# Performance work log

Hardware: AMD Instinct MI355X
Metric: run time of the kernel (lower is better)

Reference implementation:

```python
import jax, jax.numpy as jnp
import numpy as np

EPS = 1e-6
DELTA = 1e-6
GAMMA = 1.0


def setup_inputs() -> dict:
    key = jax.random.key(0)
    ks = jax.random.split(key, 6)
    B, N, D, DDIR, DSIM = 2, 384, 256, 128, 64
    sc = lambda d: 1.0 / np.sqrt(d)
    return {
        "t": jax.random.normal(ks[0], (B, N, D), jnp.float32),
        "Qd": jax.random.normal(ks[1], (D, DDIR), jnp.float32) * sc(D),
        "Kd": jax.random.normal(ks[2], (D, DDIR), jnp.float32) * sc(D),
        "Vd": jax.random.normal(ks[3], (DDIR, D), jnp.float32) * sc(DDIR),
        "Qs": jax.random.normal(ks[4], (D, DSIM), jnp.float32) * sc(D),
        "Ks": jax.random.normal(ks[5], (D, DSIM), jnp.float32) * sc(D),
        "a_l": jnp.ones((1,), jnp.float32),
        "b_l": jnp.zeros((1,), jnp.float32),
    }


def reference(t, Qd, Kd, Vd, Qs, Ks, a_l, b_l):
    B, N, D = t.shape
    d_sim = Qs.shape[1]
    # --- similarity: s_ij = <Qs t_i, Ks t_j>/sqrt(d_sim), then symmetrize ---
    q = t @ Qs  # (B,N,d_sim)
    k = t @ Ks
    s = jnp.einsum('bnd,bmd->bnm', q, k) / jnp.sqrt(jnp.float32(d_sim))
    s = 0.5 * (s + s.transpose(0, 2, 1))
    # --- global z-score over off-diagonal entries (biased var) ---
    eye = jnp.eye(N, dtype=bool)[None]  # (1,N,N)
    cnt = jnp.float32(N * (N - 1))
    mu = jnp.where(eye, 0.0, s).sum((1, 2), keepdims=True) / cnt  # (B,1,1)
    var = jnp.where(eye, 0.0, (s - mu) ** 2).sum((1, 2), keepdims=True) / cnt
    s_hat = (s - mu) / jnp.sqrt(var + EPS)
    tilde_s = a_l.reshape(-1, 1, 1) * s_hat + b_l.reshape(-1, 1, 1)
    # --- gates / mass / inertia / apportioned step ---
    A = jax.nn.sigmoid(tilde_s)                                  # (B,N,N)
    m = 1.0 / (jnp.exp(GAMMA * tilde_s).sum(axis=2) + EPS)       # (B,N)
    w = A * m[:, None, :]                                        # w_ij = m_j A_ij
    alpha = A * (w / (w.sum(axis=2, keepdims=True) + DELTA))     # (B,N,N)
    # --- antisymmetric Hadamard direction gate ---
    qd = t @ Qd  # (B,N,d_dir)
    kd = t @ Kd
    had = qd[:, :, None, :] * kd[:, None, :, :]                  # (B,N,N,d_dir)
    kappa = jnp.einsum('bijr,rd->bijd', had, Vd)                 # (B,N,N,D)
    gate = jax.nn.sigmoid(kappa - kappa.transpose(0, 2, 1, 3))
    Dpair = gate * (t[:, :, None, :] - t[:, None, :, :])         # D_ij = gate*(t_i - t_j)
    # --- exclude self pairs, aggregate update ---
    off = ~eye  # (1,N,N)
    alpha = jnp.where(off, alpha, 0.0)
    Dpair = jnp.where(off[..., None], Dpair, 0.0)
    t_next = t - jnp.einsum('bnm,bnmd->bnd', alpha, Dpair)
    return t_next
```

## Files before the change

### kernel.cpp

```cpp
#include <hip/hip_runtime.h>

#define Bn 2
#define Nn 384
#define Dn 256
#define Rn 128
#define Sn 64
#define BNn (Bn*Nn)
#define NEG_LOG2E -1.44269504088896f

typedef short short8 __attribute__((ext_vector_type(8)));
typedef float f32x4 __attribute__((ext_vector_type(4)));
typedef unsigned int uint;
typedef unsigned short ushort;

static __device__ __forceinline__ float fast_sigmoid(float x) {
    return __builtin_amdgcn_rcpf(1.0f + __expf(-x));
}
static __device__ __forceinline__ ushort f2bf(float f) {
    uint u = __float_as_uint(f);
    uint r = (u + 0x7fffu + ((u >> 16) & 1u)) >> 16;
    return (ushort)r;
}
static __device__ __forceinline__ float bf2f(ushort u) {
    return __uint_as_float(((uint)u) << 16);
}

__global__ __launch_bounds__(256)
void prep_kernel(const float* __restrict__ t,
                 const float* __restrict__ Qd, const float* __restrict__ Kd,
                 const float* __restrict__ Vd,
                 const float* __restrict__ Qs, const float* __restrict__ Ks,
                 float* __restrict__ q, float* __restrict__ k,
                 ushort* __restrict__ qdb, ushort* __restrict__ kdb,
                 ushort* __restrict__ VdT, float* __restrict__ stats) {
    const int bi = blockIdx.x;
    const int tid = threadIdx.x;
    if (bi >= 192) {
        const int idx = (bi - 192) * 256 + tid;
        const int d = idx >> 7, r = idx & 127;
        VdT[idx] = f2bf(NEG_LOG2E * Vd[(size_t)r * Dn + d]);
        if (bi == 319 && tid < 4) stats[tid] = 0.0f;
        return;
    }
    __shared__ float trow[4][Dn];
    const int r0 = bi * 4;
    for (int idx = tid; idx < 4 * Dn; idx += 256)
        trow[idx >> 8][idx & 255] = t[(size_t)r0 * Dn + idx];
    __syncthreads();
    {
        const float* W = (tid < 128) ? Qd : Kd;
        ushort* ob = (tid < 128) ? qdb : kdb;
        const int col = tid & 127;
        float a0 = 0.f, a1 = 0.f, a2 = 0.f, a3 = 0.f;
        for (int kk = 0; kk < Dn; kk += 4) {
            float4 t0 = *(const float4*)&trow[0][kk];
            float4 t1 = *(const float4*)&trow[1][kk];
            float4 t2 = *(const float4*)&trow[2][kk];
            float4 t3 = *(const float4*)&trow[3][kk];
            float w0 = W[(size_t)(kk + 0) * 128 + col];
            float w1 = W[(size_t)(kk + 1) * 128 + col];
            float w2 = W[(size_t)(kk + 2) * 128 + col];
            float w3 = W[(size_t)(kk + 3) * 128 + col];
            a0 += t0.x * w0 + t0.y * w1 + t0.z * w2 + t0.w * w3;
            a1 += t1.x * w0 + t1.y * w1 + t1.z * w2 + t1.w * w3;
            a2 += t2.x * w0 + t2.y * w1 + t2.z * w2 + t2.w * w3;
            a3 += t3.x * w0 + t3.y * w1 + t3.z * w2 + t3.w * w3;
        }
        ob[(size_t)(r0 + 0) * 128 + col] = f2bf(a0);
        ob[(size_t)(r0 + 1) * 128 + col] = f2bf(a1);
        ob[(size_t)(r0 + 2) * 128 + col] = f2bf(a2);
        ob[(size_t)(r0 + 3) * 128 + col] = f2bf(a3);
    }
    if (tid < 128) {
        const float* W = (tid < 64) ? Qs : Ks;
        float* of = (tid < 64) ? q : k;
        const int col = tid & 63;
        float a0 = 0.f, a1 = 0.f, a2 = 0.f, a3 = 0.f;
        for (int kk = 0; kk < Dn; kk += 4) {
            float4 t0 = *(const float4*)&trow[0][kk];
            float4 t1 = *(const float4*)&trow[1][kk];
            float4 t2 = *(const float4*)&trow[2][kk];
            float4 t3 = *(const float4*)&trow[3][kk];
            float w0 = W[(size_t)(kk + 0) * 64 + col];
            float w1 = W[(size_t)(kk + 1) * 64 + col];
            float w2 = W[(size_t)(kk + 2) * 64 + col];
            float w3 = W[(size_t)(kk + 3) * 64 + col];
            a0 += t0.x * w0 + t0.y * w1 + t0.z * w2 + t0.w * w3;
            a1 += t1.x * w0 + t1.y * w1 + t1.z * w2 + t1.w * w3;
            a2 += t2.x * w0 + t2.y * w1 + t2.z * w2 + t2.w * w3;
            a3 += t3.x * w0 + t3.y * w1 + t3.z * w2 + t3.w * w3;
        }
        of[(size_t)(r0 + 0) * 64 + col] = a0;
        of[(size_t)(r0 + 1) * 64 + col] = a1;
        of[(size_t)(r0 + 2) * 64 + col] = a2;
        of[(size_t)(r0 + 3) * 64 + col] = a3;
    }
}

__global__ __launch_bounds__(256)
void ssym_kernel(const float* __restrict__ q, const float* __restrict__ k,
                 float* __restrict__ ssym, float* __restrict__ stats) {
    __shared__ float qi[16][68], ki[16][68], qj[16][68], kj[16][68];
    __shared__ float red[256];
    const int b = blockIdx.z, it = blockIdx.x, jt = blockIdx.y;
    const int tid = threadIdx.x;
    const int r0 = tid >> 6, c = tid & 63;
#pragma unroll
    for (int p = 0; p < 4; ++p) {
        int row = r0 + 4 * p;
        qi[row][c] = q[((size_t)(b * Nn + it * 16 + row)) * Sn + c];
        ki[row][c] = k[((size_t)(b * Nn + it * 16 + row)) * Sn + c];
        qj[row][c] = q[((size_t)(b * Nn + jt * 16 + row)) * Sn + c];
        kj[row][c] = k[((size_t)(b * Nn + jt * 16 + row)) * Sn + c];
    }
    __syncthreads();
    const int ti = tid >> 4, tj = tid & 15;
    float acc = 0.0f;
#pragma unroll
    for (int dd = 0; dd < Sn; dd += 4) {
        float4 a  = *(const float4*)&qi[ti][dd];
        float4 bb = *(const float4*)&kj[tj][dd];
        float4 cc = *(const float4*)&qj[tj][dd];
        float4 d  = *(const float4*)&ki[ti][dd];
        acc += a.x * bb.x + a.y * bb.y + a.z * bb.z + a.w * bb.w
             + cc.x * d.x + cc.y * d.y + cc.z * d.z + cc.w * d.w;
    }
    const float sval = acc * 0.0625f;
    const int gi = it * 16 + ti, gj = jt * 16 + tj;
    ssym[((size_t)(b * Nn + gi)) * Nn + gj] = sval;
    const float v = (gi == gj) ? 0.0f : sval;

    red[tid] = v;
    __syncthreads();
    for (int off = 128; off > 0; off >>= 1) {
        if (tid < off) red[tid] += red[tid + off];
        __syncthreads();
    }
    const float tot_s = red[0];
    __syncthreads();
    red[tid] = v * v;
    __syncthreads();
    for (int off = 128; off > 0; off >>= 1) {
        if (tid < off) red[tid] += red[tid + off];
        __syncthreads();
    }
    if (tid == 0) {
        atomicAdd(&stats[b * 2 + 0], tot_s);
        atomicAdd(&stats[b * 2 + 1], red[0]);
    }
}

__global__ __launch_bounds__(256)
void m_kernel(const float* __restrict__ ssym, const float* __restrict__ stats,
              const float* __restrict__ a_l, const float* __restrict__ b_l,
              const float* __restrict__ t, float* __restrict__ out,
              float* __restrict__ m) {
    __shared__ float red[256];
    const int row = blockIdx.x;
    const int b = row / Nn;
    const float cnt_inv = 1.0f / (float)(Nn * (Nn - 1));
    const float mu = stats[b * 2 + 0] * cnt_inv;
    const float var = stats[b * 2 + 1] * cnt_inv - mu * mu;
    const float isg = rsqrtf(var + 1e-6f);
    const float a = a_l[0], bbias = b_l[0];
    const int tid = threadIdx.x;
    out[(size_t)row * Dn + tid] = t[(size_t)row * Dn + tid];
    float sum = __expf(a * (ssym[(size_t)row * Nn + tid] - mu) * isg + bbias);
    if (tid < 128)
        sum += __expf(a * (ssym[(size_t)row * Nn + 256 + tid] - mu) * isg + bbias);
    red[tid] = sum;
    __syncthreads();
    for (int off = 128; off > 0; off >>= 1) {
        if (tid < off) red[tid] += red[tid + off];
        __syncthreads();
    }
    if (tid == 0) m[row] = 1.0f / (red[0] + 1e-6f);
}

__global__ __launch_bounds__(256, 3)
void pair_kernel(const float* __restrict__ t, const float* __restrict__ ssym,
                 const float* __restrict__ mptr, const float* __restrict__ stats,
                 const float* __restrict__ a_l, const float* __restrict__ b_l,
                 const ushort* __restrict__ qdb, const ushort* __restrict__ kdb,
                 const ushort* __restrict__ VdT, float* __restrict__ out) {
    __shared__ ushort h_s[128][136];
    __shared__ float alpha_s[Nn];
    __shared__ float qdi_s[Rn], kdi_s[Rn];
    __shared__ float red[256];

    const int bx = blockIdx.x;
    const int tile = bx / BNn;
    const int bi = bx - tile * BNn;
    const int jt0 = tile * 128;
    const int b = bi / Nn;
    const int i = bi - b * Nn;
    const int tid = threadIdx.x;
    const int wave = tid >> 6, lane = tid & 63;
    const int ln = lane & 15, quad = lane >> 4;
    const int wd0 = wave * 64;

    if (tid < Rn) {
        qdi_s[tid] = bf2f(qdb[(size_t)bi * Rn + tid]);
        kdi_s[tid] = bf2f(kdb[(size_t)bi * Rn + tid]);
    }

    {
        const float cnt_inv = 1.0f / (float)(Nn * (Nn - 1));
        const float mu = stats[b * 2 + 0] * cnt_inv;
        const float var = stats[b * 2 + 1] * cnt_inv - mu * mu;
        const float isg = rsqrtf(var + 1e-6f);
        const float a = a_l[0], bbias = b_l[0];
        float A0, am0, A1 = 0.f, am1 = 0.f;
        {
            float s0 = ssym[(size_t)bi * Nn + tid];
            A0 = fast_sigmoid(a * (s0 - mu) * isg + bbias);
            am0 = A0 * mptr[b * Nn + tid];
        }
        if (tid < 128) {
            float s1 = ssym[(size_t)bi * Nn + 256 + tid];
            A1 = fast_sigmoid(a * (s1 - mu) * isg + bbias);
            am1 = A1 * mptr[b * Nn + 256 + tid];
        }
        red[tid] = am0 + am1;
        __syncthreads();
        for (int off = 128; off > 0; off >>= 1) {
            if (tid < off) red[tid] += red[tid + off];
            __syncthreads();
        }
        const float inv = 1.0f / (red[0] + 1e-6f);
        alpha_s[tid] = (tid == i) ? 0.f : A0 * am0 * inv;
        if (tid < 128)
            alpha_s[256 + tid] = ((256 + tid) == i) ? 0.f : A1 * am1 * inv;
    }

    {
        const int jj = tid >> 1;
        const int r0s = (tid & 1) * 64;
        const size_t rowj = (size_t)(b * Nn + jt0 + jj) * Rn;
        const uint4* qp = (const uint4*)(qdb + rowj + r0s);
        const uint4* kp = (const uint4*)(kdb + rowj + r0s);
#pragma unroll
        for (int c = 0; c < 8; ++c) {
            uint4 qv = qp[c], kv = kp[c];
            uint pk[4];
#pragma unroll
            for (int p = 0; p < 4; ++p) {
                uint qu = (&qv.x)[p], ku = (&kv.x)[p];
                float qlo = __uint_as_float(qu << 16);
                float qhi = __uint_as_float(qu & 0xffff0000u);
                float klo = __uint_as_float(ku << 16);
                float khi = __uint_as_float(ku & 0xffff0000u);
                const int r = r0s + c * 8 + p * 2;
                float h0 = qdi_s[r]     * klo - kdi_s[r]     * qlo;
                float h1 = qdi_s[r + 1] * khi - kdi_s[r + 1] * qhi;
                pk[p] = (uint)f2bf(h0) | ((uint)f2bf(h1) << 16);
            }
            uint4 w; w.x = pk[0]; w.y = pk[1]; w.z = pk[2]; w.w = pk[3];
            *(uint4*)&h_s[jj][r0s + c * 8] = w;
        }
    }

    short8 vf[4][4];
#pragma unroll
    for (int dt = 0; dt < 4; ++dt)
#pragma unroll
        for (int ks = 0; ks < 4; ++ks)
            vf[dt][ks] = *(const short8*)&VdT[(size_t)(wd0 + dt * 16 + ln) * Rn + ks * 32 + quad * 8];

    float4 tiv[4];
#pragma unroll
    for (int dt = 0; dt < 4; ++dt)
        tiv[dt] = *(const float4*)&t[(size_t)bi * Dn + wd0 + dt * 16 + quad * 4];

    float4 outac[4];
#pragma unroll
    for (int dt = 0; dt < 4; ++dt) outac[dt] = make_float4(0.f, 0.f, 0.f, 0.f);

    __syncthreads();

#pragma unroll 1
    for (int jsub = 0; jsub < 8; ++jsub) {
        short8 hf[4];
#pragma unroll
        for (int ks = 0; ks < 4; ++ks)
            hf[ks] = *(const short8*)&h_s[jsub * 16 + ln][ks * 32 + quad * 8];
        const int j = jt0 + jsub * 16 + ln;
        const float al = alpha_s[j];
        const size_t trow_ = (size_t)(b * Nn + j) * Dn;
        float4 tjv[4];
#pragma unroll
        for (int dt = 0; dt < 4; ++dt)
            tjv[dt] = *(const float4*)&t[trow_ + wd0 + dt * 16 + quad * 4];

        f32x4 aA[4], aB[4];
#pragma unroll
        for (int dt = 0; dt < 4; ++dt) {
            f32x4 x = {0.f, 0.f, 0.f, 0.f}, y = {0.f, 0.f, 0.f, 0.f};
            x = __builtin_amdgcn_mfma_f32_16x16x32_bf16(vf[dt][0], hf[0], x, 0, 0, 0);
            y = __builtin_amdgcn_mfma_f32_16x16x32_bf16(vf[dt][1], hf[1], y, 0, 0, 0);
            x = __builtin_amdgcn_mfma_f32_16x16x32_bf16(vf[dt][2], hf[2], x, 0, 0, 0);
            y = __builtin_amdgcn_mfma_f32_16x16x32_bf16(vf[dt][3], hf[3], y, 0, 0, 0);
            aA[dt] = x; aB[dt] = y;
        }
#pragma unroll
        for (int dt = 0; dt < 4; ++dt) {
            const float4 tj = tjv[dt];
            float e0 = aA[dt][0] + aB[dt][0];
            float e1 = aA[dt][1] + aB[dt][1];
            float e2 = aA[dt][2] + aB[dt][2];
            float e3 = aA[dt][3] + aB[dt][3];
            float g0 = __builtin_amdgcn_rcpf(1.0f + __builtin_amdgcn_exp2f(e0));
            float g1 = __builtin_amdgcn_rcpf(1.0f + __builtin_amdgcn_exp2f(e1));
            float g2 = __builtin_amdgcn_rcpf(1.0f + __builtin_amdgcn_exp2f(e2));
            float g3 = __builtin_amdgcn_rcpf(1.0f + __builtin_amdgcn_exp2f(e3));
            outac[dt].x += al * g0 * (tiv[dt].x - tj.x);
            outac[dt].y += al * g1 * (tiv[dt].y - tj.y);
            outac[dt].z += al * g2 * (tiv[dt].z - tj.z);
            outac[dt].w += al * g3 * (tiv[dt].w - tj.w);
        }
    }

#pragma unroll
    for (int dt = 0; dt < 4; ++dt) {
        float4 v = outac[dt];
#pragma unroll
        for (int mask = 1; mask < 16; mask <<= 1) {
            v.x += __shfl_xor(v.x, mask);
            v.y += __shfl_xor(v.y, mask);
            v.z += __shfl_xor(v.z, mask);
            v.w += __shfl_xor(v.w, mask);
        }
        if (ln == 0) {
            float* op = &out[(size_t)bi * Dn + wd0 + dt * 16 + quad * 4];
            atomicAdd(op + 0, -v.x);
            atomicAdd(op + 1, -v.y);
            atomicAdd(op + 2, -v.z);
            atomicAdd(op + 3, -v.w);
        }
    }
}

extern "C" void kernel_launch(void* const* d_in, const int* in_sizes, int n_in,
                              void* d_out, int out_size, void* d_ws, size_t ws_size,
                              hipStream_t stream) {
    const float* t   = (const float*)d_in[0];
    const float* Qd  = (const float*)d_in[1];
    const float* Kd  = (const float*)d_in[2];
    const float* Vd  = (const float*)d_in[3];
    const float* Qs  = (const float*)d_in[4];
    const float* Ks  = (const float*)d_in[5];
    const float* a_l = (const float*)d_in[6];
    const float* b_l = (const float*)d_in[7];
    float* out = (float*)d_out;
    float* ws  = (float*)d_ws;

    float* q     = ws;
    float* k     = q + BNn * Sn;
    float* ssym  = k + BNn * Sn;
    float* m     = ssym + (size_t)BNn * Nn;
    float* stats = m + BNn;
    ushort* qdb  = (ushort*)(stats + 8);
    ushort* kdb  = qdb + (size_t)BNn * Rn;
    ushort* VdT  = kdb + (size_t)BNn * Rn;

    hipLaunchKernelGGL(prep_kernel, dim3(320), dim3(256), 0, stream,
                       t, Qd, Kd, Vd, Qs, Ks, q, k, qdb, kdb, VdT, stats);
    hipLaunchKernelGGL(ssym_kernel, dim3(Nn / 16, Nn / 16, Bn), dim3(256), 0, stream,
                       q, k, ssym, stats);
    hipLaunchKernelGGL(m_kernel, dim3(BNn), dim3(256), 0, stream,
                       ssym, stats, a_l, b_l, t, out, m);
    hipLaunchKernelGGL(pair_kernel, dim3(3 * BNn), dim3(256), 0, stream,
                       t, ssym, m, stats, a_l, b_l, qdb, kdb, VdT, out);
}
```

Before: 191.9 us.

## Precompute alpha row denominators in separate kernel and halve pair-kernel j-tile

Adds a wden_kernel that computes each row's inverse normalizer of sum_j A_ij m_j once, instead of every pair-kernel block recomputing the full 384-wide row reduction. The pair kernel then computes alpha only for its own 64-column tile. The tile shrinks from 128 to 64 columns, giving twice as many blocks with less shared memory and a higher occupancy hint. The cost is an extra kernel launch and reloading the per-block i-row state (VdT fragments, t_i) across twice as many blocks.

```diff
diff --git a/kernel.cpp b/kernel.cpp
--- a/kernel.cpp
+++ b/kernel.cpp
@@ -177,21 +177,54 @@
     if (tid == 0) m[row] = 1.0f / (red[0] + 1e-6f);
 }
 
-__global__ __launch_bounds__(256, 3)
+__global__ __launch_bounds__(256)
+void wden_kernel(const float* __restrict__ ssym, const float* __restrict__ stats,
+                 const float* __restrict__ a_l, const float* __restrict__ b_l,
+                 const float* __restrict__ m, float* __restrict__ invden) {
+    __shared__ float red[256];
+    const int row = blockIdx.x;
+    const int b = row / Nn;
+    const float cnt_inv = 1.0f / (float)(Nn * (Nn - 1));
+    const float mu = stats[b * 2 + 0] * cnt_inv;
+    const float var = stats[b * 2 + 1] * cnt_inv - mu * mu;
+    const float isg = rsqrtf(var + 1e-6f);
+    const float a = a_l[0], bbias = b_l[0];
+    const int tid = threadIdx.x;
+    float wsum;
+    {
+        float s0 = ssym[(size_t)row * Nn + tid];
+        float A0 = fast_sigmoid(a * (s0 - mu) * isg + bbias);
+        wsum = A0 * m[b * Nn + tid];
+    }
+    if (tid < 128) {
+        float s1 = ssym[(size_t)row * Nn + 256 + tid];
+        float A1 = fast_sigmoid(a * (s1 - mu) * isg + bbias);
+        wsum += A1 * m[b * Nn + 256 + tid];
+    }
+    red[tid] = wsum;
+    __syncthreads();
+    for (int off = 128; off > 0; off >>= 1) {
+        if (tid < off) red[tid] += red[tid + off];
+        __syncthreads();
+    }
+    if (tid == 0) invden[row] = 1.0f / (red[0] + 1e-6f);
+}
+
+__global__ __launch_bounds__(256, 6)
 void pair_kernel(const float* __restrict__ t, const float* __restrict__ ssym,
                  const float* __restrict__ mptr, const float* __restrict__ stats,
                  const float* __restrict__ a_l, const float* __restrict__ b_l,
+                 const float* __restrict__ invden,
                  const ushort* __restrict__ qdb, const ushort* __restrict__ kdb,
                  const ushort* __restrict__ VdT, float* __restrict__ out) {
-    __shared__ ushort h_s[128][136];
-    __shared__ float alpha_s[Nn];
+    __shared__ ushort h_s[64][136];
+    __shared__ float alpha_s[64];
     __shared__ float qdi_s[Rn], kdi_s[Rn];
-    __shared__ float red[256];
 
     const int bx = blockIdx.x;
     const int tile = bx / BNn;
     const int bi = bx - tile * BNn;
-    const int jt0 = tile * 128;
+    const int jt0 = tile * 64;
     const int b = bi / Nn;
     const int i = bi - b * Nn;
     const int tid = threadIdx.x;
@@ -203,44 +236,29 @@
         qdi_s[tid] = bf2f(qdb[(size_t)bi * Rn + tid]);
         kdi_s[tid] = bf2f(kdb[(size_t)bi * Rn + tid]);
     }
-
-    {
+    if (tid >= 192) {
+        const int jl = tid - 192;
+        const int j = jt0 + jl;
         const float cnt_inv = 1.0f / (float)(Nn * (Nn - 1));
         const float mu = stats[b * 2 + 0] * cnt_inv;
         const float var = stats[b * 2 + 1] * cnt_inv - mu * mu;
         const float isg = rsqrtf(var + 1e-6f);
         const float a = a_l[0], bbias = b_l[0];
-        float A0, am0, A1 = 0.f, am1 = 0.f;
-        {
-            float s0 = ssym[(size_t)bi * Nn + tid];
-            A0 = fast_sigmoid(a * (s0 - mu) * isg + bbias);
-            am0 = A0 * mptr[b * Nn + tid];
-        }
-        if (tid < 128) {
-            float s1 = ssym[(size_t)bi * Nn + 256 + tid];
-            A1 = fast_sigmoid(a * (s1 - mu) * isg + bbias);
-            am1 = A1 * mptr[b * Nn + 256 + tid];
-        }
-        red[tid] = am0 + am1;
-        __syncthreads();
-        for (int off = 128; off > 0; off >>= 1) {
-            if (tid < off) red[tid] += red[tid + off];
-            __syncthreads();
-        }
-        const float inv = 1.0f / (red[0] + 1e-6f);
-        alpha_s[tid] = (tid == i) ? 0.f : A0 * am0 * inv;
-        if (tid < 128)
-            alpha_s[256 + tid] = ((256 + tid) == i) ? 0.f : A1 * am1 * inv;
-    }
+        float s = ssym[(size_t)bi * Nn + j];
+        float A = fast_sigmoid(a * (s - mu) * isg + bbias);
+        float al = A * A * mptr[b * Nn + j] * invden[bi];
+        alpha_s[jl] = (j == i) ? 0.f : al;
+    }
+    __syncthreads();
 
     {
-        const int jj = tid >> 1;
-        const int r0s = (tid & 1) * 64;
+        const int jj = tid >> 2;
+        const int r0s = (tid & 3) * 32;
         const size_t rowj = (size_t)(b * Nn + jt0 + jj) * Rn;
         const uint4* qp = (const uint4*)(qdb + rowj + r0s);
         const uint4* kp = (const uint4*)(kdb + rowj + r0s);
 #pragma unroll
-        for (int c = 0; c < 8; ++c) {
+        for (int c = 0; c < 4; ++c) {
             uint4 qv = qp[c], kv = kp[c];
             uint pk[4];
 #pragma unroll
@@ -279,13 +297,13 @@
     __syncthreads();
 
 #pragma unroll 1
-    for (int jsub = 0; jsub < 8; ++jsub) {
+    for (int jsub = 0; jsub < 4; ++jsub) {
         short8 hf[4];
 #pragma unroll
         for (int ks = 0; ks < 4; ++ks)
             hf[ks] = *(const short8*)&h_s[jsub * 16 + ln][ks * 32 + quad * 8];
         const int j = jt0 + jsub * 16 + ln;
-        const float al = alpha_s[j];
+        const float al = alpha_s[jsub * 16 + ln];
         const size_t trow_ = (size_t)(b * Nn + j) * Dn;
         float4 tjv[4];
 #pragma unroll
@@ -354,14 +372,15 @@
     float* out = (float*)d_out;
     float* ws  = (float*)d_ws;
 
-    float* q     = ws;
-    float* k     = q + BNn * Sn;
-    float* ssym  = k + BNn * Sn;
-    float* m     = ssym + (size_t)BNn * Nn;
-    float* stats = m + BNn;
-    ushort* qdb  = (ushort*)(stats + 8);
-    ushort* kdb  = qdb + (size_t)BNn * Rn;
-    ushort* VdT  = kdb + (size_t)BNn * Rn;
+    float* q      = ws;
+    float* k      = q + BNn * Sn;
+    float* ssym   = k + BNn * Sn;
+    float* m      = ssym + (size_t)BNn * Nn;
+    float* invden = m + BNn;
+    float* stats  = invden + BNn;
+    ushort* qdb   = (ushort*)(stats + 8);
+    ushort* kdb   = qdb + (size_t)BNn * Rn;
+    ushort* VdT   = kdb + (size_t)BNn * Rn;
 
     hipLaunchKernelGGL(prep_kernel, dim3(320), dim3(256), 0, stream,
                        t, Qd, Kd, Vd, Qs, Ks, q, k, qdb, kdb, VdT, stats);
@@ -369,6 +388,8 @@
                        q, k, ssym, stats);
     hipLaunchKernelGGL(m_kernel, dim3(BNn), dim3(256), 0, stream,
                        ssym, stats, a_l, b_l, t, out, m);
-    hipLaunchKernelGGL(pair_kernel, dim3(3 * BNn), dim3(256), 0, stream,
-                       t, ssym, m, stats, a_l, b_l, qdb, kdb, VdT, out);
-}
+    hipLaunchKernelGGL(wden_kernel, dim3(BNn), dim3(256), 0, stream,
+                       ssym, stats, a_l, b_l, m, invden);
+    hipLaunchKernelGGL(pair_kernel, dim3(6 * BNn), dim3(256), 0, stream,
+                       t, ssym, m, stats, a_l, b_l, invden, qdb, kdb, VdT, out);
+}
```

Result: slower. 367.3 us (+91.5%).
